# Optimization experiments

Hardware: AMD Instinct MI355X
Metric: run time of the kernel (lower is better)

The kernel has to match this reference:

```python
import jax, jax.numpy as jnp
import numpy as np

DIM = 768
NUM_HEADS = 12
HEAD_DIM = DIM // NUM_HEADS
B, QLEN, KVLEN = 8, 512, 4096


def setup_inputs() -> dict:
    key = jax.random.key(0)
    ks = jax.random.split(key, 12)
    s = 1.0 / np.sqrt(DIM)
    return {
        "query": jax.random.normal(ks[0], (B, QLEN, DIM), jnp.float32),
        "key": jax.random.normal(ks[1], (B, KVLEN, DIM), jnp.float32),
        "value": jax.random.normal(ks[2], (B, KVLEN, DIM), jnp.float32),
        "attention_mask": jax.random.randint(ks[3], (B, QLEN, KVLEN), 0, 2, jnp.int32),
        "Wq": jax.random.normal(ks[4], (DIM, DIM), jnp.float32) * s,
        "bq": jnp.zeros((DIM,), jnp.float32),
        "Wk": jax.random.normal(ks[5], (DIM, DIM), jnp.float32) * s,
        "bk": jnp.zeros((DIM,), jnp.float32),
        "Wv": jax.random.normal(ks[6], (DIM, DIM), jnp.float32) * s,
        "bv": jnp.zeros((DIM,), jnp.float32),
        "Wo": jax.random.normal(ks[7], (DIM, DIM), jnp.float32) * s,
        "bo": jnp.zeros((DIM,), jnp.float32),
        "ln_g": jnp.ones((DIM,), jnp.float32),
        "ln_b": jnp.zeros((DIM,), jnp.float32),
    }


def _layer_norm(x, g, b, eps=1e-5):
    mu = jnp.mean(x, axis=-1, keepdims=True)
    var = jnp.var(x, axis=-1, keepdims=True)
    return (x - mu) * jax.lax.rsqrt(var + eps) * g + b


def reference(query, key, value, attention_mask, Wq, bq, Wk, bk, Wv, bv, Wo, bo, ln_g, ln_b):
    # LayerNorm on query only (as in original), then QKV projections
    q = _layer_norm(query, ln_g, ln_b)
    q = q @ Wq.T + bq                      # [B, Q, D]
    k = key @ Wk.T + bk                    # [B, KV, D]
    v = value @ Wv.T + bv                  # [B, KV, D]

    # split heads: [B, H, S, Dh]
    q = q.reshape(B, QLEN, NUM_HEADS, HEAD_DIM).transpose(0, 2, 1, 3)
    k = k.reshape(B, KVLEN, NUM_HEADS, HEAD_DIM).transpose(0, 2, 1, 3)
    v = v.reshape(B, KVLEN, NUM_HEADS, HEAD_DIM).transpose(0, 2, 1, 3)

    scale = HEAD_DIM ** -0.5
    scores = jnp.einsum("bhqd,bhkd->bhqk", q, k) * scale  # [B, H, Q, KV]
    mask = (attention_mask == 1)[:, None, :, :]            # broadcast over heads
    scores = jnp.where(mask, -jnp.inf, scores)
    attn = jax.nn.softmax(scores, axis=-1)
    # dropout layers are identity in eval mode
    out = jnp.einsum("bhqk,bhkd->bhqd", attn, v)           # [B, H, Q, Dh]
    out = out.transpose(0, 2, 1, 3).reshape(B, QLEN, DIM)
    out = out @ Wo.T + bo
    return out
```

## Files before the change

kernel.cpp:

```cpp
#include <hip/hip_runtime.h>
#include <hip/hip_bf16.h>

typedef __bf16 bf16;
typedef bf16 bf16x8 __attribute__((ext_vector_type(8)));
typedef bf16 bf16x4 __attribute__((ext_vector_type(4)));
typedef bf16 bf16x2 __attribute__((ext_vector_type(2)));
typedef short s16x4 __attribute__((ext_vector_type(4)));
typedef float f32x4 __attribute__((ext_vector_type(4)));

#define NB 8
#define QLEN 512
#define KVL 4096
#define DIM 768
#define NH 12
#define HD 64

#if __has_builtin(__builtin_amdgcn_mfma_f32_16x16x16_bf16)
static __device__ __forceinline__ f32x4 pv16(bf16x4 a, bf16x4 b, f32x4 c) {
  return __builtin_amdgcn_mfma_f32_16x16x16_bf16(a, b, c, 0, 0, 0);
}
#else
static __device__ __forceinline__ f32x4 pv16(bf16x4 a, bf16x4 b, f32x4 c) {
  return __builtin_amdgcn_mfma_f32_16x16x16bf16_1k(
      __builtin_bit_cast(s16x4, a), __builtin_bit_cast(s16x4, b), c, 0, 0, 0);
}
#endif

__global__ __launch_bounds__(256) void ln_q(const float* __restrict__ x,
    const float* __restrict__ g, const float* __restrict__ beta,
    bf16* __restrict__ out)
{
  int row  = blockIdx.x * 4 + (threadIdx.x >> 6);
  int lane = threadIdx.x & 63;
  const float* rp = x + (size_t)row * DIM;
  f32x4 v[3];
  float s = 0.f, s2 = 0.f;
#pragma unroll
  for (int i = 0; i < 3; ++i) {
    v[i] = *reinterpret_cast<const f32x4*>(rp + (i * 64 + lane) * 4);
#pragma unroll
    for (int j = 0; j < 4; ++j) { s += v[i][j]; s2 += v[i][j] * v[i][j]; }
  }
#pragma unroll
  for (int o = 1; o < 64; o <<= 1) { s += __shfl_xor(s, o); s2 += __shfl_xor(s2, o); }
  float mean = s * (1.f / 768.f);
  float var  = s2 * (1.f / 768.f) - mean * mean;
  float rstd = rsqrtf(var + 1e-5f);
#pragma unroll
  for (int i = 0; i < 3; ++i) {
    int c = (i * 64 + lane) * 4;
    f32x4 gg = *reinterpret_cast<const f32x4*>(g + c);
    f32x4 bb = *reinterpret_cast<const f32x4*>(beta + c);
    bf16x4 o4;
#pragma unroll
    for (int j = 0; j < 4; ++j) o4[j] = (bf16)((v[i][j] - mean) * rstd * gg[j] + bb[j]);
    *reinterpret_cast<bf16x4*>(out + (size_t)row * DIM + c) = o4;
  }
}

__global__ __launch_bounds__(256) void pack_mask(const int* __restrict__ m,
                                                 unsigned* __restrict__ bits)
{
  const int total = NB * QLEN * KVL;
  int stride = gridDim.x * blockDim.x;
  for (int i = blockIdx.x * blockDim.x + threadIdx.x; i < total; i += stride) {
    unsigned long long bal = __ballot(m[i] == 1);
    int lane = threadIdx.x & 63;
    if ((lane & 31) == 0)
      bits[i >> 5] = (unsigned)(bal >> (lane & 32));
  }
}

__global__ __launch_bounds__(256) void conv_w(
    const float* __restrict__ w0, const float* __restrict__ w1,
    const float* __restrict__ w2, const float* __restrict__ w3,
    bf16* __restrict__ o0, bf16* __restrict__ o1,
    bf16* __restrict__ o2, bf16* __restrict__ o3)
{
  int sel = blockIdx.y;
  const float* s = sel == 0 ? w0 : sel == 1 ? w1 : sel == 2 ? w2 : w3;
  bf16* d = sel == 0 ? o0 : sel == 1 ? o1 : sel == 2 ? o2 : o3;
  int i = (blockIdx.x * 256 + threadIdx.x) * 8;
  f32x4 a = *reinterpret_cast<const f32x4*>(s + i);
  f32x4 b = *reinterpret_cast<const f32x4*>(s + i + 4);
  bf16x8 v;
#pragma unroll
  for (int j = 0; j < 4; ++j) { v[j] = (bf16)a[j]; v[4 + j] = (bf16)b[j]; }
  *reinterpret_cast<bf16x8*>(d + i) = v;
}

template<bool A_IS_BF16, bool OUT_BF16>
__global__ __launch_bounds__(256) void gemm128(const void* __restrict__ Aptr,
    const bf16* __restrict__ W, const float* __restrict__ bias,
    void* __restrict__ Out)
{
  const int K = 768, N = 768;
  __shared__ __align__(16) bf16 a_s[128][72];
  __shared__ __align__(16) bf16 b_s[128][72];
  int raw = blockIdx.x;
  int nt = (raw >> 3) % 6;
  int mt = ((raw >> 3) / 6) * 8 + (raw & 7);
  int m0 = mt * 128, n0 = nt * 128;
  int tid = threadIdx.x;
  int lane = tid & 63, wid = tid >> 6;
  int l16 = lane & 15, g4 = lane >> 4;
  int wm = wid >> 1, wn = wid & 1;
  f32x4 acc[4][4] = {};

  for (int k0 = 0; k0 < K; k0 += 64) {
#pragma unroll
    for (int i = 0; i < 4; ++i) {
      int oct = tid + i * 256;
      int row = oct >> 3, col = (oct & 7) * 8;
      bf16x8 av;
      if constexpr (A_IS_BF16) {
        av = *reinterpret_cast<const bf16x8*>((const bf16*)Aptr + (size_t)(m0 + row) * K + k0 + col);
      } else {
        const float* ap = (const float*)Aptr + (size_t)(m0 + row) * K + k0 + col;
        f32x4 f0 = *reinterpret_cast<const f32x4*>(ap);
        f32x4 f1 = *reinterpret_cast<const f32x4*>(ap + 4);
#pragma unroll
        for (int j = 0; j < 4; ++j) { av[j] = (bf16)f0[j]; av[4 + j] = (bf16)f1[j]; }
      }
      *reinterpret_cast<bf16x8*>(&a_s[row][col]) = av;

      *reinterpret_cast<bf16x8*>(&b_s[row][col]) =
          *reinterpret_cast<const bf16x8*>(W + (size_t)(n0 + row) * K + k0 + col);
    }
    __syncthreads();
#pragma unroll
    for (int kk = 0; kk < 2; ++kk) {
      bf16x8 af[4], bfv[4];
#pragma unroll
      for (int mi = 0; mi < 4; ++mi)
        af[mi] = *reinterpret_cast<const bf16x8*>(&a_s[wm * 64 + mi * 16 + l16][kk * 32 + g4 * 8]);
#pragma unroll
      for (int ni = 0; ni < 4; ++ni)
        bfv[ni] = *reinterpret_cast<const bf16x8*>(&b_s[wn * 64 + ni * 16 + l16][kk * 32 + g4 * 8]);
#pragma unroll
      for (int mi = 0; mi < 4; ++mi)
#pragma unroll
        for (int ni = 0; ni < 4; ++ni)
          acc[mi][ni] = __builtin_amdgcn_mfma_f32_16x16x32_bf16(af[mi], bfv[ni], acc[mi][ni], 0, 0, 0);
    }
    __syncthreads();
  }
#pragma unroll
  for (int mi = 0; mi < 4; ++mi)
#pragma unroll
    for (int ni = 0; ni < 4; ++ni) {
      int col = n0 + wn * 64 + ni * 16 + l16;
      float bv = bias[col];
#pragma unroll
      for (int j = 0; j < 4; ++j) {
        int row = m0 + wm * 64 + mi * 16 + g4 * 4 + j;
        float v = acc[mi][ni][j] + bv;
        if constexpr (OUT_BF16) ((bf16*)Out)[(size_t)row * N + col] = (bf16)v;
        else                    ((float*)Out)[(size_t)row * N + col] = v;
      }
    }
}

__global__ __launch_bounds__(256, 4) void attn(const bf16* __restrict__ Qp,
    const bf16* __restrict__ Kp, const bf16* __restrict__ Vp,
    const unsigned* __restrict__ mbits, bf16* __restrict__ Ctx)
{
  int h = blockIdx.x, qt = blockIdx.y, b = blockIdx.z;
  int tid = threadIdx.x, lane = tid & 63, wid = tid >> 6;
  int g4 = lane >> 4, l16 = lane & 15;
  __shared__ __align__(16) bf16 k_s[2][64][72];
  __shared__ __align__(16) bf16 v_s[2][64][72];

  int qrow_w = b * QLEN + qt * 64 + wid * 16;
  int q = qrow_w + l16;

  bf16x8 qf[2];
#pragma unroll
  for (int kk = 0; kk < 2; ++kk) {
    bf16x8 t = *reinterpret_cast<const bf16x8*>(Qp + (size_t)q * DIM + h * HD + kk * 32 + g4 * 8);
#pragma unroll
    for (int j = 0; j < 8; ++j) qf[kk][j] = (bf16)((float)t[j] * 0.125f);
  }

  const bf16* Kb = Kp + (size_t)b * KVL * DIM + h * HD;
  const bf16* Vb = Vp + (size_t)b * KVL * DIM + h * HD;
  const unsigned* mrow = mbits + (size_t)q * (KVL / 32);

  f32x4 oacc[4] = {};
  float l_r = 0.f;

  int krow = tid >> 3, kcol = (tid & 7) * 8;
  int va = tid & 31, vd0 = (tid >> 5) * 8;
  int vpos = (va & 1) * 2 + (va >> 3) * 4 + ((va >> 1) & 3) * 16;

  bf16x8 kreg0, kreg1, vreg0, vreg1;
  unsigned m0w, m1w, m0n, m1n;

  kreg0 = *reinterpret_cast<const bf16x8*>(Kb + (size_t)krow * DIM + kcol);
  kreg1 = *reinterpret_cast<const bf16x8*>(Kb + (size_t)(krow + 32) * DIM + kcol);
  vreg0 = *reinterpret_cast<const bf16x8*>(Vb + (size_t)(2 * va) * DIM + vd0);
  vreg1 = *reinterpret_cast<const bf16x8*>(Vb + (size_t)(2 * va + 1) * DIM + vd0);
  m0w = mrow[0]; m1w = mrow[1];
  *reinterpret_cast<bf16x8*>(&k_s[0][krow][kcol]) = kreg0;
  *reinterpret_cast<bf16x8*>(&k_s[0][krow + 32][kcol]) = kreg1;
#pragma unroll
  for (int j = 0; j < 8; ++j) {
    bf16x2 w; w[0] = vreg0[j]; w[1] = vreg1[j];
    *reinterpret_cast<bf16x2*>(&v_s[0][vd0 + j][vpos]) = w;
  }
  __syncthreads();

  const int NT = KVL / 64;
  for (int t = 0; t < NT; ++t) {
    int buf = t & 1;
    if (t + 1 < NT) {
      int kv0n = (t + 1) * 64;
      kreg0 = *reinterpret_cast<const bf16x8*>(Kb + (size_t)(kv0n + krow) * DIM + kcol);
      kreg1 = *reinterpret_cast<const bf16x8*>(Kb + (size_t)(kv0n + krow + 32) * DIM + kcol);
      vreg0 = *reinterpret_cast<const bf16x8*>(Vb + (size_t)(kv0n + 2 * va) * DIM + vd0);
      vreg1 = *reinterpret_cast<const bf16x8*>(Vb + (size_t)(kv0n + 2 * va + 1) * DIM + vd0);
      m0n = mrow[(t + 1) * 2];
      m1n = mrow[(t + 1) * 2 + 1];
    }

    f32x4 sacc[4] = {};
#pragma unroll
    for (int nb = 0; nb < 4; ++nb)
#pragma unroll
      for (int kk = 0; kk < 2; ++kk) {
        bf16x8 kf = *reinterpret_cast<const bf16x8*>(&k_s[buf][nb * 16 + l16][kk * 32 + g4 * 8]);
        sacc[nb] = __builtin_amdgcn_mfma_f32_16x16x32_bf16(kf, qf[kk], sacc[nb], 0, 0, 0);
      }

    float p[16];
#pragma unroll
    for (int nb = 0; nb < 4; ++nb) {
      unsigned w = (nb < 2) ? m0w : m1w;
#pragma unroll
      for (int r = 0; r < 4; ++r) {
        int bit = (nb & 1) * 16 + g4 * 4 + r;
        p[nb * 4 + r] = ((w >> bit) & 1u) ? 0.f : __expf(sacc[nb][r]);
      }
    }
    float sm[8];
#pragma unroll
    for (int i = 0; i < 8; ++i) sm[i] = p[i] + p[i + 8];
#pragma unroll
    for (int i = 0; i < 4; ++i) sm[i] += sm[i + 4];
    l_r += (sm[0] + sm[1]) + (sm[2] + sm[3]);

    bf16x4 pq[4];
#pragma unroll
    for (int nb = 0; nb < 4; ++nb)
#pragma unroll
      for (int j = 0; j < 4; ++j) pq[nb][j] = (bf16)p[nb * 4 + j];

#pragma unroll
    for (int db = 0; db < 4; ++db) {
      bf16x8 vr0 = *reinterpret_cast<const bf16x8*>(&v_s[buf][db * 16 + l16][g4 * 16]);
      bf16x8 vr1 = *reinterpret_cast<const bf16x8*>(&v_s[buf][db * 16 + l16][g4 * 16 + 8]);
      oacc[db] = pv16(__builtin_shufflevector(vr0, vr0, 0, 1, 2, 3), pq[0], oacc[db]);
      oacc[db] = pv16(__builtin_shufflevector(vr0, vr0, 4, 5, 6, 7), pq[1], oacc[db]);
      oacc[db] = pv16(__builtin_shufflevector(vr1, vr1, 0, 1, 2, 3), pq[2], oacc[db]);
      oacc[db] = pv16(__builtin_shufflevector(vr1, vr1, 4, 5, 6, 7), pq[3], oacc[db]);
    }

    if (t + 1 < NT) {
      int nb2 = buf ^ 1;
      *reinterpret_cast<bf16x8*>(&k_s[nb2][krow][kcol]) = kreg0;
      *reinterpret_cast<bf16x8*>(&k_s[nb2][krow + 32][kcol]) = kreg1;
#pragma unroll
      for (int j = 0; j < 8; ++j) {
        bf16x2 w; w[0] = vreg0[j]; w[1] = vreg1[j];
        *reinterpret_cast<bf16x2*>(&v_s[nb2][vd0 + j][vpos]) = w;
      }
      m0w = m0n; m1w = m1n;
    }
    __syncthreads();
  }

  l_r += __shfl_xor(l_r, 16);
  l_r += __shfl_xor(l_r, 32);

  bf16* o_base = &k_s[0][0][0] + (size_t)wid * 16 * 72;
  float inv = 1.f / l_r;
#pragma unroll
  for (int db = 0; db < 4; ++db) {
    bf16x4 t4;
#pragma unroll
    for (int r = 0; r < 4; ++r) t4[r] = (bf16)(oacc[db][r] * inv);
    *reinterpret_cast<bf16x4*>(o_base + l16 * 72 + db * 16 + g4 * 4) = t4;
  }
#pragma unroll
  for (int pass = 0; pass < 2; ++pass) {
    int row = (lane >> 3) + pass * 8;
    int c8 = (lane & 7) * 8;
    bf16x8 v = *reinterpret_cast<const bf16x8*>(o_base + row * 72 + c8);
    *reinterpret_cast<bf16x8*>(Ctx + (size_t)(qrow_w + row) * DIM + h * HD + c8) = v;
  }
}

extern "C" void kernel_launch(void* const* d_in, const int* in_sizes, int n_in,
                              void* d_out, int out_size, void* d_ws, size_t ws_size,
                              hipStream_t stream) {
  const float* query = (const float*)d_in[0];
  const float* key   = (const float*)d_in[1];
  const float* value = (const float*)d_in[2];
  const int*   amask = (const int*)d_in[3];
  const float* Wq = (const float*)d_in[4];
  const float* bq = (const float*)d_in[5];
  const float* Wk = (const float*)d_in[6];
  const float* bk = (const float*)d_in[7];
  const float* Wv = (const float*)d_in[8];
  const float* bv = (const float*)d_in[9];
  const float* Wo = (const float*)d_in[10];
  const float* bo = (const float*)d_in[11];
  const float* ln_g = (const float*)d_in[12];
  const float* ln_b = (const float*)d_in[13];

  char* ws = (char*)d_ws;
  bf16* qln = (bf16*)ws;      ws += (size_t)NB * QLEN * DIM * 2;
  bf16* Qp  = (bf16*)ws;      ws += (size_t)NB * QLEN * DIM * 2;
  bf16* Kp  = (bf16*)ws;      ws += (size_t)NB * KVL * DIM * 2;
  bf16* Vp  = (bf16*)ws;      ws += (size_t)NB * KVL * DIM * 2;
  bf16* Ctx = (bf16*)ws;      ws += (size_t)NB * QLEN * DIM * 2;
  unsigned* mbits = (unsigned*)ws; ws += (size_t)NB * QLEN * (KVL / 32) * 4;
  bf16* Wqb = (bf16*)ws;      ws += (size_t)DIM * DIM * 2;
  bf16* Wkb = (bf16*)ws;      ws += (size_t)DIM * DIM * 2;
  bf16* Wvb = (bf16*)ws;      ws += (size_t)DIM * DIM * 2;
  bf16* Wob = (bf16*)ws;

  ln_q<<<NB * QLEN / 4, 256, 0, stream>>>(query, ln_g, ln_b, qln);
  pack_mask<<<1024, 256, 0, stream>>>(amask, mbits);
  conv_w<<<dim3(DIM * DIM / (256 * 8), 4), 256, 0, stream>>>(Wq, Wk, Wv, Wo, Wqb, Wkb, Wvb, Wob);

  gemm128<true,  true><<<(NB * QLEN / 128) * 6, 256, 0, stream>>>(qln,   Wqb, bq, Qp);
  gemm128<false, true><<<(NB * KVL  / 128) * 6, 256, 0, stream>>>(key,   Wkb, bk, Kp);
  gemm128<false, true><<<(NB * KVL  / 128) * 6, 256, 0, stream>>>(value, Wvb, bv, Vp);

  attn<<<dim3(NH, QLEN / 64, NB), 256, 0, stream>>>(Qp, Kp, Vp, mbits, Ctx);

  gemm128<true, false><<<(NB * QLEN / 128) * 6, 256, 0, stream>>>(Ctx, Wob, bo, (float*)d_out);
}
```

Before: 328.5 us.

## Load GEMM weight tiles directly into LDS with pre-swizzled layout

The weight conversion kernel now writes each bf16 row with its 8-element groups XOR-permuted by row index. The GEMM loads the B tile with global_load_lds straight into an unpadded LDS buffer, bypassing registers, and undoes the swizzle when reading fragments to avoid bank conflicts. This cuts register traffic and LDS padding for the weight operand. It relies on the weight layout and the read-side XOR matching exactly. Any other consumer of the converted weights (for example an output projection using a different kernel) would also need to account for the swizzle.

```diff
diff --git a/kernel.cpp b/kernel.cpp
--- a/kernel.cpp
+++ b/kernel.cpp
@@ -81,8 +81,12 @@
   const float* s = sel == 0 ? w0 : sel == 1 ? w1 : sel == 2 ? w2 : w3;
   bf16* d = sel == 0 ? o0 : sel == 1 ? o1 : sel == 2 ? o2 : o3;
   int i = (blockIdx.x * 256 + threadIdx.x) * 8;
-  f32x4 a = *reinterpret_cast<const f32x4*>(s + i);
-  f32x4 b = *reinterpret_cast<const f32x4*>(s + i + 4);
+  int n = i / DIM;
+  int k = i - n * DIM;
+  int ks = (k & ~63) | ((((k >> 3) ^ n) & 7) << 3);
+  const float* sp = s + (size_t)n * DIM + ks;
+  f32x4 a = *reinterpret_cast<const f32x4*>(sp);
+  f32x4 b = *reinterpret_cast<const f32x4*>(sp + 4);
   bf16x8 v;
 #pragma unroll
   for (int j = 0; j < 4; ++j) { v[j] = (bf16)a[j]; v[4 + j] = (bf16)b[j]; }
@@ -96,7 +100,7 @@
 {
   const int K = 768, N = 768;
   __shared__ __align__(16) bf16 a_s[128][72];
-  __shared__ __align__(16) bf16 b_s[128][72];
+  __shared__ __align__(16) bf16 b_s[128][64];
   int raw = blockIdx.x;
   int nt = (raw >> 3) % 6;
   int mt = ((raw >> 3) / 6) * 8 + (raw & 7);
@@ -123,9 +127,19 @@
         for (int j = 0; j < 4; ++j) { av[j] = (bf16)f0[j]; av[4 + j] = (bf16)f1[j]; }
       }
       *reinterpret_cast<bf16x8*>(&a_s[row][col]) = av;
-
-      *reinterpret_cast<bf16x8*>(&b_s[row][col]) =
-          *reinterpret_cast<const bf16x8*>(W + (size_t)(n0 + row) * K + k0 + col);
+    }
+#pragma unroll
+    for (int i = 0; i < 4; ++i) {
+      int chunk = wid * 4 + i;
+      const bf16* gp = W + (size_t)(n0 + chunk * 8 + (lane >> 3)) * K + k0 + (lane & 7) * 8;
+#if __has_builtin(__builtin_amdgcn_global_load_lds)
+      __builtin_amdgcn_global_load_lds(
+          (const __attribute__((address_space(1))) void*)gp,
+          (__attribute__((address_space(3))) void*)&b_s[chunk * 8][0], 16, 0, 0);
+#else
+      *reinterpret_cast<bf16x8*>(&b_s[chunk * 8 + (lane >> 3)][(lane & 7) * 8]) =
+          *reinterpret_cast<const bf16x8*>(gp);
+#endif
     }
     __syncthreads();
 #pragma unroll
@@ -135,8 +149,11 @@
       for (int mi = 0; mi < 4; ++mi)
         af[mi] = *reinterpret_cast<const bf16x8*>(&a_s[wm * 64 + mi * 16 + l16][kk * 32 + g4 * 8]);
 #pragma unroll
-      for (int ni = 0; ni < 4; ++ni)
-        bfv[ni] = *reinterpret_cast<const bf16x8*>(&b_s[wn * 64 + ni * 16 + l16][kk * 32 + g4 * 8]);
+      for (int ni = 0; ni < 4; ++ni) {
+        int brow = wn * 64 + ni * 16 + l16;
+        int bg = ((kk * 4 + g4) ^ (brow & 7)) * 8;
+        bfv[ni] = *reinterpret_cast<const bf16x8*>(&b_s[brow][bg]);
+      }
 #pragma unroll
       for (int mi = 0; mi < 4; ++mi)
 #pragma unroll
```

Result: no change. 329.3 us (+0.3%).
